# Kernel tuning notes

Hardware: AMD Instinct MI355X
Metric: run time of the kernel (lower is better)

## Reference

```python
import jax
jax.config.update('jax_enable_x64', True)  # hash math uses int64 like torch .long()
import jax.numpy as jnp
import numpy as np

BUCKETS = 2 ** 21
PRIMES = jnp.array([73856093, 19349669, 83492791], dtype=jnp.int64)
# 8 trilinear corner offsets, (8,3)
OFFSETS = jnp.array([[0, 0, 0], [1, 0, 0], [0, 1, 0], [1, 1, 0],
                     [0, 0, 1], [1, 0, 1], [0, 1, 1], [1, 1, 1]], dtype=jnp.int64)
# level resolutions: resolution * level_scale**(num_levels-1-lv) = [0.24, 0.12]
RES = (0.24, 0.12)


def setup_inputs() -> dict:
    key = jax.random.key(0)
    k1, k2, k3 = jax.random.split(key, 3)
    pts = jax.random.normal(k1, (262144, 3), dtype=jnp.float32)
    features0 = jax.random.normal(k2, (BUCKETS, 32), dtype=jnp.float32) * 0.01
    features1 = jax.random.normal(k3, (BUCKETS, 32), dtype=jnp.float32) * 0.01
    return {"pts": pts, "features0": features0, "features1": features1}


def _level_query(pts, feats, res):
    # torch computes grid indices under no_grad -> no gradient to pts
    q = jax.lax.stop_gradient(pts / jnp.float32(res))        # (N,3) continuous coords
    base = jnp.floor(q)                                      # (N,3)
    idx = base.astype(jnp.int64)[:, None, :] + OFFSETS[None, :, :]  # (N,8,3)
    vid = jnp.mod((idx * PRIMES).sum(-1), BUCKETS)           # (N,8) hashed bucket ids
    feat = feats[vid]                                        # (N,8,d) gather
    frac = (q - base).astype(feats.dtype)                    # (N,3)
    wx = jnp.stack([1 - frac[:, 0], frac[:, 0]], 1)
    wy = jnp.stack([1 - frac[:, 1], frac[:, 1]], 1)
    wz = jnp.stack([1 - frac[:, 2], frac[:, 2]], 1)
    w = (wx[:, [0, 1, 0, 1, 0, 1, 0, 1]]
         * wy[:, [0, 0, 1, 1, 0, 0, 1, 1]]
         * wz[:, [0, 0, 0, 0, 1, 1, 1, 1]])                  # (N,8)
    return (feat * w[:, :, None]).sum(1)                     # (N,d)


def reference(pts, features0, features1):
    per = [_level_query(pts, features0, RES[0]),
           _level_query(pts, features1, RES[1])]
    return jnp.concatenate(per, axis=-1)                     # (N, 64)
```

## Files before the change

### kernel.cpp

```cpp
#include <hip/hip_runtime.h>

#define BUCKET_MASK ((1u << 21) - 1u)

__global__ __launch_bounds__(256) void voxel_hash_kernel(
    const float* __restrict__ pts,
    const float* __restrict__ feats0,
    const float* __restrict__ feats1,
    float* __restrict__ out,
    int npts)
{
    int gid = blockIdx.x * 256 + threadIdx.x;
    int n   = gid >> 4;
    int sub = gid & 15;
    if (n >= npts) return;

    int level = sub >> 3;
    int chunk = sub & 7;

    const float res = level ? 0.12f : 0.24f;
    const float* __restrict__ feats = level ? feats1 : feats0;

    float px = pts[n * 3 + 0];
    float py = pts[n * 3 + 1];
    float pz = pts[n * 3 + 2];

    float qx = px / res, qy = py / res, qz = pz / res;
    float bx = floorf(qx), by = floorf(qy), bz = floorf(qz);
    float fx = qx - bx, fy = qy - by, fz = qz - bz;

    int ix = (int)bx, iy = (int)by, iz = (int)bz;

    unsigned hx0 = (unsigned)ix * 73856093u;
    unsigned hy0 = (unsigned)iy * 19349669u;
    unsigned hz0 = (unsigned)iz * 83492791u;
    unsigned hx1 = hx0 + 73856093u;
    unsigned hy1 = hy0 + 19349669u;
    unsigned hz1 = hz0 + 83492791u;

    float gx = 1.0f - fx, gy = 1.0f - fy, gz = 1.0f - fz;

    float4 acc = make_float4(0.0f, 0.0f, 0.0f, 0.0f);

    #pragma unroll
    for (int c = 0; c < 8; ++c) {
        unsigned h = ((c & 1) ? hx1 : hx0)
                   + ((c & 2) ? hy1 : hy0)
                   + ((c & 4) ? hz1 : hz0);
        unsigned vid = h & BUCKET_MASK;
        float w = ((c & 1) ? fx : gx) * ((c & 2) ? fy : gy) * ((c & 4) ? fz : gz);

        const float4 f = *reinterpret_cast<const float4*>(
            feats + (size_t)vid * 32u + (unsigned)chunk * 4u);
        acc.x += w * f.x;
        acc.y += w * f.y;
        acc.z += w * f.z;
        acc.w += w * f.w;
    }

    *reinterpret_cast<float4*>(out + (size_t)n * 64u + (unsigned)sub * 4u) = acc;
}

extern "C" void kernel_launch(void* const* d_in, const int* in_sizes, int n_in,
                              void* d_out, int out_size, void* d_ws, size_t ws_size,
                              hipStream_t stream) {
    const float* pts = (const float*)d_in[0];
    const float* f0  = (const float*)d_in[1];
    const float* f1  = (const float*)d_in[2];
    float* out = (float*)d_out;

    int npts = in_sizes[0] / 3;
    long long threads = (long long)npts * 16;
    int grid = (int)((threads + 255) / 256);

    voxel_hash_kernel<<<grid, 256, 0, stream>>>(pts, f0, f1, out, npts);
}
```

Measured before the change: 40.52 us.

## Split levels across grid y dimension and use nontemporal loads/stores

Assigns each hash level to its own blockIdx.y slice, so every thread block gathers from a single feature table, which may improve cache locality for the random gathers. Point loads and output stores become nontemporal to keep streaming data out of cache, leaving room for the feature tables. Each point's coordinates are now read by two separate blocks, and output rows are written as two half-row 128-byte segments instead of one full row.

Result: no change. 41.30 us (+1.9%).

```diff
diff --git a/kernel.cpp b/kernel.cpp
--- a/kernel.cpp
+++ b/kernel.cpp
@@ -1,6 +1,8 @@
 #include <hip/hip_runtime.h>
 
 #define BUCKET_MASK ((1u << 21) - 1u)
+
+typedef float f4 __attribute__((ext_vector_type(4)));
 
 __global__ __launch_bounds__(256) void voxel_hash_kernel(
     const float* __restrict__ pts,
@@ -9,20 +11,18 @@
     float* __restrict__ out,
     int npts)
 {
-    int gid = blockIdx.x * 256 + threadIdx.x;
-    int n   = gid >> 4;
-    int sub = gid & 15;
+    int level = blockIdx.y;
+    int t = blockIdx.x * 256 + threadIdx.x;
+    int n     = t >> 3;
+    int chunk = t & 7;
     if (n >= npts) return;
-
-    int level = sub >> 3;
-    int chunk = sub & 7;
 
     const float res = level ? 0.12f : 0.24f;
     const float* __restrict__ feats = level ? feats1 : feats0;
 
-    float px = pts[n * 3 + 0];
-    float py = pts[n * 3 + 1];
-    float pz = pts[n * 3 + 2];
+    float px = __builtin_nontemporal_load(pts + n * 3 + 0);
+    float py = __builtin_nontemporal_load(pts + n * 3 + 1);
+    float pz = __builtin_nontemporal_load(pts + n * 3 + 2);
 
     float qx = px / res, qy = py / res, qz = pz / res;
     float bx = floorf(qx), by = floorf(qy), bz = floorf(qz);
@@ -39,7 +39,7 @@
 
     float gx = 1.0f - fx, gy = 1.0f - fy, gz = 1.0f - fz;
 
-    float4 acc = make_float4(0.0f, 0.0f, 0.0f, 0.0f);
+    f4 acc = (f4)(0.0f);
 
     #pragma unroll
     for (int c = 0; c < 8; ++c) {
@@ -49,15 +49,14 @@
         unsigned vid = h & BUCKET_MASK;
         float w = ((c & 1) ? fx : gx) * ((c & 2) ? fy : gy) * ((c & 4) ? fz : gz);
 
-        const float4 f = *reinterpret_cast<const float4*>(
+        const f4 f = *reinterpret_cast<const f4*>(
             feats + (size_t)vid * 32u + (unsigned)chunk * 4u);
-        acc.x += w * f.x;
-        acc.y += w * f.y;
-        acc.z += w * f.z;
-        acc.w += w * f.w;
+        acc += w * f;
     }
 
-    *reinterpret_cast<float4*>(out + (size_t)n * 64u + (unsigned)sub * 4u) = acc;
+    f4* dst = reinterpret_cast<f4*>(
+        out + (size_t)n * 64u + (unsigned)level * 32u + (unsigned)chunk * 4u);
+    __builtin_nontemporal_store(acc, dst);
 }
 
 extern "C" void kernel_launch(void* const* d_in, const int* in_sizes, int n_in,
@@ -69,8 +68,9 @@
     float* out = (float*)d_out;
 
     int npts = in_sizes[0] / 3;
-    long long threads = (long long)npts * 16;
-    int grid = (int)((threads + 255) / 256);
+    long long threads = (long long)npts * 8;
+    int gx = (int)((threads + 255) / 256);
+    dim3 grid(gx, 2, 1);
 
     voxel_hash_kernel<<<grid, 256, 0, stream>>>(pts, f0, f1, out, npts);
 }
```
